# Optimization experiments

Hardware: AMD Instinct MI355X
Metric: run time of the kernel (lower is better)

The kernel has to match this reference:

```python
import jax, jax.numpy as jnp
import numpy as np

NEG_SLOPE = 0.2  # PyG GATv2Conv default negative_slope


def gatv2_conv(x, src, dst, Wl, bl, Wr, br, att, bias, concat=True):
    # x: [N, Fin]; src/dst: [E] (message flows src -> dst, softmax over dst)
    N = x.shape[0]
    H, C = att.shape
    xl = (x @ Wl + bl).reshape(N, H, C)  # source-side transform (lin_l)
    xr = (x @ Wr + br).reshape(N, H, C)  # target-side transform (lin_r)
    e = xl[src] + xr[dst]                              # [E, H, C]
    score = jnp.sum(jax.nn.leaky_relu(e, NEG_SLOPE) * att, axis=-1)  # [E, H]
    # segment softmax over incoming edges of each target node
    m = jax.ops.segment_max(score, dst, num_segments=N)               # [N, H]
    a = jnp.exp(score - m[dst])
    denom = jax.ops.segment_sum(a, dst, num_segments=N)               # [N, H]
    alpha = a / denom[dst]                                            # [E, H]
    out = jax.ops.segment_sum(xl[src] * alpha[..., None], dst, num_segments=N)  # [N, H, C]
    if concat:
        out = out.reshape(N, H * C)
    else:
        out = out.mean(axis=1)
    return out + bias


def setup_inputs() -> dict:
    key = jax.random.key(0)
    ks = jax.random.split(key, 12)
    N, E, Fin = 100000, 1600000, 128
    H1, C1 = 8, 16
    C2 = 64
    def glorot(k, shape):
        fan_in, fan_out = shape[0], shape[-1]
        lim = (6.0 / (fan_in + fan_out)) ** 0.5
        return jax.random.uniform(k, shape, jnp.float32, -lim, lim)
    x = jax.random.normal(ks[0], (N, Fin), jnp.float32)
    edge_index = jax.random.randint(ks[1], (2, E), 0, N, dtype=jnp.int64)
    return {
        "x": x,
        "edge_index": edge_index,
        "Wl1": glorot(ks[2], (Fin, H1 * C1)),
        "bl1": jnp.zeros((H1 * C1,), jnp.float32),
        "Wr1": glorot(ks[3], (Fin, H1 * C1)),
        "br1": jnp.zeros((H1 * C1,), jnp.float32),
        "att1": glorot(ks[4], (H1, C1)),
        "bias1": jnp.zeros((H1 * C1,), jnp.float32),
        "Wl2": glorot(ks[5], (H1 * C1, C2)),
        "bl2": jnp.zeros((C2,), jnp.float32),
        "Wr2": glorot(ks[6], (H1 * C1, C2)),
        "br2": jnp.zeros((C2,), jnp.float32),
        "att2": glorot(ks[7], (1, C2)),
        "bias2": jnp.zeros((C2,), jnp.float32),
    }


def reference(x, edge_index, Wl1, bl1, Wr1, br1, att1, bias1,
              Wl2, bl2, Wr2, br2, att2, bias2):
    N = x.shape[0]
    loops = jnp.arange(N, dtype=edge_index.dtype)
    src = jnp.concatenate([edge_index[0], loops])  # PyG adds self loops by default
    dst = jnp.concatenate([edge_index[1], loops])
    # eval mode: F.dropout(training=False) is identity
    h = gatv2_conv(x, src, dst, Wl1, bl1, Wr1, br1, att1, bias1, concat=True)
    h = jax.nn.elu(h)
    out = gatv2_conv(h, src, dst, Wl2, bl2, Wr2, br2, att2, bias2, concat=True)
    return out
```

## Files before the change

### kernel.cpp

```cpp
#include <hip/hip_runtime.h>
#include <math.h>

#define FIN 128
#define F1  128
#define C2  64
#define NEG 0.2f

#define BKT_SHIFT 8
#define BKT_SIZE  256
#define SCAT_CHUNK 8192
#define IMGCAP 8192

typedef _Float16 half4 __attribute__((ext_vector_type(4)));
typedef _Float16 f16x8 __attribute__((ext_vector_type(8)));
typedef _Float16 h2    __attribute__((ext_vector_type(2)));
typedef float    f32x4 __attribute__((ext_vector_type(4)));

union H8u { f16x8 v; h2 p[4]; };

__device__ __forceinline__ float lrelu(float z) { return fmaxf(z, NEG * z); }

__global__ __launch_bounds__(256) void bucket_hist_kernel(
    const int* __restrict__ ei, int* __restrict__ bcnt, int E, int ET, int NBKT) {
  __shared__ int sh[512];
  const int t = threadIdx.x;
  for (int b = t; b < NBKT; b += 256) sh[b] = 0;
  __syncthreads();
  const int g0 = blockIdx.x * SCAT_CHUNK + t;
#pragma unroll
  for (int i = 0; i < 32; ++i) {
    const int g = g0 + i * 256;
    if (g < ET) {
      const int dst = (g < E) ? ei[E + g] : (g - E);
      atomicAdd(&sh[dst >> BKT_SHIFT], 1);
    }
  }
  __syncthreads();
  for (int b = t; b < NBKT; b += 256)
    if (sh[b]) atomicAdd(&bcnt[b], sh[b]);
}

__global__ __launch_bounds__(512) void bucket_scan_kernel(
    const int* __restrict__ bcnt, int* __restrict__ bbase, int* __restrict__ bcur,
    int* __restrict__ indptr, int NBKT, int N, int ET) {
  __shared__ int sh[512];
  const int t = threadIdx.x;
  const int v = (t < NBKT) ? bcnt[t] : 0;
  sh[t] = v;
  __syncthreads();
  for (int off = 1; off < 512; off <<= 1) {
    int val = (t >= off) ? sh[t - off] : 0;
    __syncthreads();
    sh[t] += val;
    __syncthreads();
  }
  const int excl = sh[t] - v;
  if (t < NBKT) { bbase[t] = excl; bcur[t] = excl; }
  if (t == NBKT - 1) bbase[NBKT] = excl + v;
  if (t == 0) indptr[N] = ET;
}

__global__ __launch_bounds__(256) void bucket_scatter_kernel(
    const int* __restrict__ ei, int* __restrict__ bcur, int* __restrict__ tmp,
    int E, int ET, int NBKT) {
  __shared__ int sh_hist[512];
  __shared__ int sh_base[512];
  const int t = threadIdx.x;
  for (int b = t; b < NBKT; b += 256) sh_hist[b] = 0;
  __syncthreads();
  const int g0 = blockIdx.x * SCAT_CHUNK + t;
  int bk[32], pk[32];
#pragma unroll
  for (int i = 0; i < 32; ++i) {
    const int g = g0 + i * 256;
    int b = -1, p = 0;
    if (g < ET) {
      const int src = (g < E) ? ei[g] : (g - E);
      const int dst = (g < E) ? ei[E + g] : (g - E);
      b = dst >> BKT_SHIFT;
      p = (src << BKT_SHIFT) | (dst & (BKT_SIZE - 1));
      atomicAdd(&sh_hist[b], 1);
    }
    bk[i] = b; pk[i] = p;
  }
  __syncthreads();
  for (int b = t; b < NBKT; b += 256) {
    const int c = sh_hist[b];
    sh_base[b] = c ? atomicAdd(&bcur[b], c) : 0;
    sh_hist[b] = 0;
  }
  __syncthreads();
#pragma unroll
  for (int i = 0; i < 32; ++i) {
    if (bk[i] >= 0) {
      const int off = atomicAdd(&sh_hist[bk[i]], 1);
      tmp[sh_base[bk[i]] + off] = pk[i];
    }
  }
}

__global__ __launch_bounds__(256) void build_csr_kernel(
    const int* __restrict__ tmp, const int* __restrict__ bbase,
    int* __restrict__ indptr, int* __restrict__ csr, int N) {
  __shared__ int cnt[256];
  __shared__ int cur[256];
  __shared__ int img[IMGCAP];
  const int b = blockIdx.x;
  const int t = threadIdx.x;
  const int base = bbase[b];
  const int cntb = bbase[b + 1] - base;
  cnt[t] = 0;
  __syncthreads();
  for (int i = t; i < cntb; i += 256)
    atomicAdd(&cnt[tmp[base + i] & (BKT_SIZE - 1)], 1);
  __syncthreads();
  const int v = cnt[t];
  cur[t] = v;
  __syncthreads();
  for (int off = 1; off < 256; off <<= 1) {
    int val = (t >= off) ? cur[t - off] : 0;
    __syncthreads();
    cur[t] += val;
    __syncthreads();
  }
  const int excl = cur[t] - v;
  const int node = (b << BKT_SHIFT) + t;
  if (node < N) indptr[node] = base + excl;
  __syncthreads();
  cur[t] = excl;
  __syncthreads();
  if (cntb <= IMGCAP) {
    for (int i = t; i < cntb; i += 256) {
      const int p = tmp[base + i];
      const int pos = atomicAdd(&cur[p & (BKT_SIZE - 1)], 1);
      img[pos] = p >> BKT_SHIFT;
    }
    __syncthreads();
    for (int i = t; i < cntb; i += 256) csr[base + i] = img[i];
  } else {
    for (int i = t; i < cntb; i += 256) {
      const int p = tmp[base + i];
      const int pos = atomicAdd(&cur[p & (BKT_SIZE - 1)], 1);
      csr[base + pos] = p >> BKT_SHIFT;
    }
  }
}

__global__ __launch_bounds__(256) void conv_fp16_kernel(
    const float* __restrict__ src, _Float16* __restrict__ dst, int n4) {
  const int i = blockIdx.x * 256 + threadIdx.x;
  if (i < n4) {
    const float4 v = ((const float4*)src)[i];
    half4 h;
    h.x = (_Float16)v.x; h.y = (_Float16)v.y;
    h.z = (_Float16)v.z; h.w = (_Float16)v.w;
    ((half4*)dst)[i] = h;
  }
}

__global__ __launch_bounds__(256) void wtrans_kernel(
    const float* __restrict__ W0, const float* __restrict__ W1,
    const float* __restrict__ W2, const float* __restrict__ W3,
    _Float16* __restrict__ T0, _Float16* __restrict__ T1,
    _Float16* __restrict__ T2, _Float16* __restrict__ T3) {
  const int m = blockIdx.y;
  const float* W = (m == 0) ? W0 : (m == 1) ? W1 : (m == 2) ? W2 : W3;
  _Float16* T = (m == 0) ? T0 : (m == 1) ? T1 : (m == 2) ? T2 : T3;
  const int ncols = (m < 2) ? 128 : 64;
  const int idx = blockIdx.x * 256 + threadIdx.x;
  if (idx < ncols * 128) {
    const int n = idx >> 7;
    const int k = idx & 127;
    T[idx] = (_Float16)W[k * ncols + n];
  }
}

template<int NCOLS, int CPW>
__global__ __launch_bounds__(256) void gemm_mfma_kernel(
    const _Float16* __restrict__ A,
    const _Float16* __restrict__ Wt0, const float* __restrict__ b0, _Float16* __restrict__ O0,
    const _Float16* __restrict__ Wt1, const float* __restrict__ b1, _Float16* __restrict__ O1,
    int M) {
  const int zsel = blockIdx.z;
  const _Float16* Wt = zsel ? Wt1 : Wt0;
  const float* bias  = zsel ? b1 : b0;
  _Float16* O        = zsel ? O1 : O0;
  const int wave = threadIdx.x >> 6;
  const int lane = threadIdx.x & 63;
  const int row16 = lane & 15;
  const int quad  = lane >> 4;
  const int kb = quad * 8;
  f16x8 bfrag[CPW][4];
  float bv[CPW];
#pragma unroll
  for (int c = 0; c < CPW; ++c) {
    const int n0 = (wave * CPW + c) * 16;
    bv[c] = bias[n0 + row16];
#pragma unroll
    for (int kt = 0; kt < 4; ++kt)
      bfrag[c][kt] = *(const f16x8*)(Wt + (n0 + row16) * 128 + kt * 32 + kb);
  }
  const int rowTiles = (M + 15) >> 4;
  for (int rt = blockIdx.x; rt < rowTiles; rt += gridDim.x) {
    const int r0 = rt << 4;
    const int arow = min(r0 + row16, M - 1);
    f16x8 afrag[4];
#pragma unroll
    for (int kt = 0; kt < 4; ++kt)
      afrag[kt] = *(const f16x8*)(A + (size_t)arow * 128 + kt * 32 + kb);
    f32x4 acc[CPW];
#pragma unroll
    for (int c = 0; c < CPW; ++c) acc[c] = (f32x4){0.f, 0.f, 0.f, 0.f};
#pragma unroll
    for (int kt = 0; kt < 4; ++kt)
#pragma unroll
      for (int c = 0; c < CPW; ++c)
        acc[c] = __builtin_amdgcn_mfma_f32_16x16x32_f16(afrag[kt], bfrag[c][kt], acc[c], 0, 0, 0);
#pragma unroll
    for (int c = 0; c < CPW; ++c) {
      const int col = (wave * CPW + c) * 16 + row16;
#pragma unroll
      for (int r = 0; r < 4; ++r) {
        const int row = r0 + quad * 4 + r;
        if (row < M)
          O[(size_t)row * NCOLS + col] = (_Float16)(acc[c][r] + bv[c]);
      }
    }
  }
}

__global__ __launch_bounds__(256) void attn1_kernel(
    const _Float16* __restrict__ xl, const _Float16* __restrict__ xr,
    const float* __restrict__ att, const float* __restrict__ bias,
    const int* __restrict__ indptr, const int* __restrict__ csr,
    _Float16* __restrict__ hout, int N) {
  const int lane = threadIdx.x & 15;
  const int v = blockIdx.x * 16 + (threadIdx.x >> 4);
  if (v >= N) return;
  const int c8 = lane << 3;
  const _Float16* xlp = xl + c8;
  H8u xru; xru.v = *(const f16x8*)(xr + (v << 7) + c8);
  H8u atu;
  {
    const float4 a0 = *(const float4*)(att + c8);
    const float4 a1 = *(const float4*)(att + c8 + 4);
    f16x8 a;
    a[0] = (_Float16)a0.x; a[1] = (_Float16)a0.y; a[2] = (_Float16)a0.z; a[3] = (_Float16)a0.w;
    a[4] = (_Float16)a1.x; a[5] = (_Float16)a1.y; a[6] = (_Float16)a1.z; a[7] = (_Float16)a1.w;
    atu.v = a;
  }
  const h2 neg2 = {(_Float16)NEG, (_Float16)NEG};
  const h2 zero2 = {(_Float16)0.f, (_Float16)0.f};
  const int beg = indptr[v];
  const int end = indptr[v + 1];
  float l = 0.f;
  float acc[8] = {0.f, 0.f, 0.f, 0.f, 0.f, 0.f, 0.f, 0.f};
  int e = beg;
  for (; e + 4 <= end; e += 4) {
    const int s0 = csr[e + 0];
    const int s1 = csr[e + 1];
    const int s2 = csr[e + 2];
    const int s3 = csr[e + 3];
    H8u x0, x1, x2, x3;
    x0.v = *(const f16x8*)(xlp + (s0 << 7));
    x1.v = *(const f16x8*)(xlp + (s1 << 7));
    x2.v = *(const f16x8*)(xlp + (s2 << 7));
    x3.v = *(const f16x8*)(xlp + (s3 << 7));
    h2 sa0 = zero2, sa1 = zero2, sa2 = zero2, sa3 = zero2;
#pragma unroll
    for (int j = 0; j < 4; ++j) {
      h2 e0 = x0.p[j] + xru.p[j];
      h2 e1 = x1.p[j] + xru.p[j];
      h2 e2 = x2.p[j] + xru.p[j];
      h2 e3 = x3.p[j] + xru.p[j];
      e0 = __builtin_elementwise_max(e0, e0 * neg2);
      e1 = __builtin_elementwise_max(e1, e1 * neg2);
      e2 = __builtin_elementwise_max(e2, e2 * neg2);
      e3 = __builtin_elementwise_max(e3, e3 * neg2);
      sa0 = e0 * atu.p[j] + sa0;
      sa1 = e1 * atu.p[j] + sa1;
      sa2 = e2 * atu.p[j] + sa2;
      sa3 = e3 * atu.p[j] + sa3;
    }
    float t0 = (float)sa0[0] + (float)sa0[1];
    float t1 = (float)sa1[0] + (float)sa1[1];
    float t2 = (float)sa2[0] + (float)sa2[1];
    float t3 = (float)sa3[0] + (float)sa3[1];
    t0 += __shfl_xor(t0, 1);  t1 += __shfl_xor(t1, 1);
    t2 += __shfl_xor(t2, 1);  t3 += __shfl_xor(t3, 1);
    const float p0 = __expf(t0);
    const float p1 = __expf(t1);
    const float p2 = __expf(t2);
    const float p3 = __expf(t3);
    l += (p0 + p1) + (p2 + p3);
#pragma unroll
    for (int j = 0; j < 4; ++j) {
      acc[2*j]   = fmaf(p0, (float)x0.p[j][0], acc[2*j]);
      acc[2*j+1] = fmaf(p0, (float)x0.p[j][1], acc[2*j+1]);
      acc[2*j]   = fmaf(p1, (float)x1.p[j][0], acc[2*j]);
      acc[2*j+1] = fmaf(p1, (float)x1.p[j][1], acc[2*j+1]);
      acc[2*j]   = fmaf(p2, (float)x2.p[j][0], acc[2*j]);
      acc[2*j+1] = fmaf(p2, (float)x2.p[j][1], acc[2*j+1]);
      acc[2*j]   = fmaf(p3, (float)x3.p[j][0], acc[2*j]);
      acc[2*j+1] = fmaf(p3, (float)x3.p[j][1], acc[2*j+1]);
    }
  }
  for (; e < end; ++e) {
    const int s = csr[e];
    H8u xv; xv.v = *(const f16x8*)(xlp + (s << 7));
    h2 sa = zero2;
#pragma unroll
    for (int j = 0; j < 4; ++j) {
      h2 ev = xv.p[j] + xru.p[j];
      ev = __builtin_elementwise_max(ev, ev * neg2);
      sa = ev * atu.p[j] + sa;
    }
    float tt = (float)sa[0] + (float)sa[1];
    tt += __shfl_xor(tt, 1);
    const float p = __expf(tt);
    l += p;
#pragma unroll
    for (int j = 0; j < 4; ++j) {
      acc[2*j]   = fmaf(p, (float)xv.p[j][0], acc[2*j]);
      acc[2*j+1] = fmaf(p, (float)xv.p[j][1], acc[2*j+1]);
    }
  }
  const float rl = 1.f / l;
  const float4 b0 = *(const float4*)(bias + c8);
  const float4 b1 = *(const float4*)(bias + c8 + 4);
  float r[8];
  r[0] = fmaf(acc[0], rl, b0.x); r[1] = fmaf(acc[1], rl, b0.y);
  r[2] = fmaf(acc[2], rl, b0.z); r[3] = fmaf(acc[3], rl, b0.w);
  r[4] = fmaf(acc[4], rl, b1.x); r[5] = fmaf(acc[5], rl, b1.y);
  r[6] = fmaf(acc[6], rl, b1.z); r[7] = fmaf(acc[7], rl, b1.w);
  f16x8 hres;
#pragma unroll
  for (int i = 0; i < 8; ++i) {
    const float z = r[i] > 0.f ? r[i] : expm1f(r[i]);
    hres[i] = (_Float16)z;
  }
  *(f16x8*)(hout + (v << 7) + c8) = hres;
}

__global__ __launch_bounds__(256) void attn2_kernel(
    const _Float16* __restrict__ xl, const _Float16* __restrict__ xr,
    const float* __restrict__ att, const float* __restrict__ bias,
    const int* __restrict__ indptr, const int* __restrict__ csr,
    float* __restrict__ out, int N) {
  const int lane = threadIdx.x & 7;
  const int v = blockIdx.x * 32 + (threadIdx.x >> 3);
  if (v >= N) return;
  const int c8 = lane << 3;
  const _Float16* xlp = xl + c8;
  H8u xru; xru.v = *(const f16x8*)(xr + (v << 6) + c8);
  H8u atu;
  {
    const float4 a0 = *(const float4*)(att + c8);
    const float4 a1 = *(const float4*)(att + c8 + 4);
    f16x8 a;
    a[0] = (_Float16)a0.x; a[1] = (_Float16)a0.y; a[2] = (_Float16)a0.z; a[3] = (_Float16)a0.w;
    a[4] = (_Float16)a1.x; a[5] = (_Float16)a1.y; a[6] = (_Float16)a1.z; a[7] = (_Float16)a1.w;
    atu.v = a;
  }
  const h2 neg2 = {(_Float16)NEG, (_Float16)NEG};
  const h2 zero2 = {(_Float16)0.f, (_Float16)0.f};
  const int beg = indptr[v];
  const int end = indptr[v + 1];
  float l = 0.f;
  float acc[8] = {0.f, 0.f, 0.f, 0.f, 0.f, 0.f, 0.f, 0.f};
  int e = beg;
  for (; e + 4 <= end; e += 4) {
    const int s0 = csr[e + 0];
    const int s1 = csr[e + 1];
    const int s2 = csr[e + 2];
    const int s3 = csr[e + 3];
    H8u x0, x1, x2, x3;
    x0.v = *(const f16x8*)(xlp + (s0 << 6));
    x1.v = *(const f16x8*)(xlp + (s1 << 6));
    x2.v = *(const f16x8*)(xlp + (s2 << 6));
    x3.v = *(const f16x8*)(xlp + (s3 << 6));
    h2 sa0 = zero2, sa1 = zero2, sa2 = zero2, sa3 = zero2;
#pragma unroll
    for (int j = 0; j < 4; ++j) {
      h2 e0 = x0.p[j] + xru.p[j];
      h2 e1 = x1.p[j] + xru.p[j];
      h2 e2 = x2.p[j] + xru.p[j];
      h2 e3 = x3.p[j] + xru.p[j];
      e0 = __builtin_elementwise_max(e0, e0 * neg2);
      e1 = __builtin_elementwise_max(e1, e1 * neg2);
      e2 = __builtin_elementwise_max(e2, e2 * neg2);
      e3 = __builtin_elementwise_max(e3, e3 * neg2);
      sa0 = e0 * atu.p[j] + sa0;
      sa1 = e1 * atu.p[j] + sa1;
      sa2 = e2 * atu.p[j] + sa2;
      sa3 = e3 * atu.p[j] + sa3;
    }
    float t0 = (float)sa0[0] + (float)sa0[1];
    float t1 = (float)sa1[0] + (float)sa1[1];
    float t2 = (float)sa2[0] + (float)sa2[1];
    float t3 = (float)sa3[0] + (float)sa3[1];
    t0 += __shfl_xor(t0, 1);  t1 += __shfl_xor(t1, 1);
    t2 += __shfl_xor(t2, 1);  t3 += __shfl_xor(t3, 1);
    t0 += __shfl_xor(t0, 2);  t1 += __shfl_xor(t1, 2);
    t2 += __shfl_xor(t2, 2);  t3 += __shfl_xor(t3, 2);
    t0 += __shfl_xor(t0, 4);  t1 += __shfl_xor(t1, 4);
    t2 += __shfl_xor(t2, 4);  t3 += __shfl_xor(t3, 4);
    const float p0 = __expf(t0);
    const float p1 = __expf(t1);
    const float p2 = __expf(t2);
    const float p3 = __expf(t3);
    l += (p0 + p1) + (p2 + p3);
#pragma unroll
    for (int j = 0; j < 4; ++j) {
      acc[2*j]   = fmaf(p0, (float)x0.p[j][0], acc[2*j]);
      acc[2*j+1] = fmaf(p0, (float)x0.p[j][1], acc[2*j+1]);
      acc[2*j]   = fmaf(p1, (float)x1.p[j][0], acc[2*j]);
      acc[2*j+1] = fmaf(p1, (float)x1.p[j][1], acc[2*j+1]);
      acc[2*j]   = fmaf(p2, (float)x2.p[j][0], acc[2*j]);
      acc[2*j+1] = fmaf(p2, (float)x2.p[j][1], acc[2*j+1]);
      acc[2*j]   = fmaf(p3, (float)x3.p[j][0], acc[2*j]);
      acc[2*j+1] = fmaf(p3, (float)x3.p[j][1], acc[2*j+1]);
    }
  }
  for (; e < end; ++e) {
    const int s = csr[e];
    H8u xv; xv.v = *(const f16x8*)(xlp + (s << 6));
    h2 sa = zero2;
#pragma unroll
    for (int j = 0; j < 4; ++j) {
      h2 ev = xv.p[j] + xru.p[j];
      ev = __builtin_elementwise_max(ev, ev * neg2);
      sa = ev * atu.p[j] + sa;
    }
    float tt = (float)sa[0] + (float)sa[1];
    tt += __shfl_xor(tt, 1);
    tt += __shfl_xor(tt, 2);
    tt += __shfl_xor(tt, 4);
    const float p = __expf(tt);
    l += p;
#pragma unroll
    for (int j = 0; j < 4; ++j) {
      acc[2*j]   = fmaf(p, (float)xv.p[j][0], acc[2*j]);
      acc[2*j+1] = fmaf(p, (float)xv.p[j][1], acc[2*j+1]);
    }
  }
  const float rl = 1.f / l;
  const float4 b0 = *(const float4*)(bias + c8);
  const float4 b1 = *(const float4*)(bias + c8 + 4);
  float4 o0, o1;
  o0.x = fmaf(acc[0], rl, b0.x); o0.y = fmaf(acc[1], rl, b0.y);
  o0.z = fmaf(acc[2], rl, b0.z); o0.w = fmaf(acc[3], rl, b0.w);
  o1.x = fmaf(acc[4], rl, b1.x); o1.y = fmaf(acc[5], rl, b1.y);
  o1.z = fmaf(acc[6], rl, b1.z); o1.w = fmaf(acc[7], rl, b1.w);
  *(float4*)(out + (v << 6) + c8) = o0;
  *(float4*)(out + (v << 6) + c8 + 4) = o1;
}

extern "C" void kernel_launch(void* const* d_in, const int* in_sizes, int n_in,
                              void* d_out, int out_size, void* d_ws, size_t ws_size,
                              hipStream_t stream) {
  const float* x     = (const float*)d_in[0];
  const int*   ei    = (const int*)d_in[1];
  const float* Wl1   = (const float*)d_in[2];
  const float* bl1   = (const float*)d_in[3];
  const float* Wr1   = (const float*)d_in[4];
  const float* br1   = (const float*)d_in[5];
  const float* att1  = (const float*)d_in[6];
  const float* bias1 = (const float*)d_in[7];
  const float* Wl2   = (const float*)d_in[8];
  const float* bl2   = (const float*)d_in[9];
  const float* Wr2   = (const float*)d_in[10];
  const float* br2   = (const float*)d_in[11];
  const float* att2  = (const float*)d_in[12];
  const float* bias2 = (const float*)d_in[13];

  const int N  = in_sizes[0] / FIN;
  const int E  = in_sizes[1] / 2;
  const int ET = E + N;
  const int NBKT = (N + BKT_SIZE - 1) >> BKT_SHIFT;

  _Float16* xh    = (_Float16*)d_ws;
  _Float16* xl1h  = xh + (size_t)N * FIN;
  _Float16* xr1h  = xl1h + (size_t)N * F1;
  _Float16* hbufh = xr1h + (size_t)N * F1;
  _Float16* Wt1l  = hbufh + (size_t)N * F1;
  _Float16* Wt1r  = Wt1l + 128 * 128;
  _Float16* Wt2l  = Wt1r + 128 * 128;
  _Float16* Wt2r  = Wt2l + 64 * 128;
  int* indptr = (int*)(Wt2r + 64 * 128);
  int* csr    = indptr + (N + 1);
  int* bcnt   = csr + ET;
  int* bbase  = bcnt + 512;
  int* bcur   = bbase + 513;
  int* tmp    = (int*)hbufh;
  _Float16* xl2h = xl1h;
  _Float16* xr2h = xr1h;
  float* out  = (float*)d_out;

  const int sblocks = (ET + SCAT_CHUNK - 1) / SCAT_CHUNK;

  hipMemsetAsync(bcnt, 0, 512 * sizeof(int), stream);
  bucket_hist_kernel<<<sblocks, 256, 0, stream>>>(ei, bcnt, E, ET, NBKT);
  bucket_scan_kernel<<<1, 512, 0, stream>>>(bcnt, bbase, bcur, indptr, NBKT, N, ET);
  bucket_scatter_kernel<<<sblocks, 256, 0, stream>>>(ei, bcur, tmp, E, ET, NBKT);
  build_csr_kernel<<<NBKT, 256, 0, stream>>>(tmp, bbase, indptr, csr, N);

  const int n4 = N * FIN / 4;
  conv_fp16_kernel<<<(n4 + 255) / 256, 256, 0, stream>>>(x, xh, n4);
  wtrans_kernel<<<dim3(64, 4), 256, 0, stream>>>(Wl1, Wr1, Wl2, Wr2, Wt1l, Wt1r, Wt2l, Wt2r);

  gemm_mfma_kernel<128, 2><<<dim3(1024, 1, 2), 256, 0, stream>>>(
      xh, Wt1l, bl1, xl1h, Wt1r, br1, xr1h, N);

  attn1_kernel<<<(N + 15) / 16, 256, 0, stream>>>(xl1h, xr1h, att1, bias1, indptr, csr, hbufh, N);

  gemm_mfma_kernel<64, 1><<<dim3(1024, 1, 2), 256, 0, stream>>>(
      hbufh, Wt2l, bl2, xl2h, Wt2r, br2, xr2h, N);

  attn2_kernel<<<(N + 31) / 32, 256, 0, stream>>>(xl2h, xr2h, att2, bias2, indptr, csr, out, N);
}
```

Baseline: 358.9 us.

## Fuse fp32-to-fp16 conversion into GEMM, merge prep kernels, unroll attention by 8

The separate x-to-fp16 conversion kernel is removed. The first GEMM now loads fp32 rows and converts them in registers, which avoids writing and re-reading an fp16 copy of x. The weight transpose is merged into the bucket histogram kernel to save a launch. The attention kernels gain an 8-edge unrolled loop so more gathers are in flight, and they round the partial score to fp16 before the shuffle. The first GEMM now reads twice the bytes of A, and the wider unroll raises register pressure.

```diff
diff --git a/kernel.cpp b/kernel.cpp
--- a/kernel.cpp
+++ b/kernel.cpp
@@ -18,26 +18,40 @@
 
 union H8u { f16x8 v; h2 p[4]; };
 
-__device__ __forceinline__ float lrelu(float z) { return fmaxf(z, NEG * z); }
-
-__global__ __launch_bounds__(256) void bucket_hist_kernel(
-    const int* __restrict__ ei, int* __restrict__ bcnt, int E, int ET, int NBKT) {
-  __shared__ int sh[512];
+__global__ __launch_bounds__(256) void prep_kernel(
+    const int* __restrict__ ei, int* __restrict__ bcnt, int E, int ET, int NBKT, int sblocks,
+    const float* __restrict__ W0, const float* __restrict__ W1,
+    const float* __restrict__ W2, const float* __restrict__ W3,
+    _Float16* __restrict__ T0, _Float16* __restrict__ T1,
+    _Float16* __restrict__ T2, _Float16* __restrict__ T3) {
   const int t = threadIdx.x;
-  for (int b = t; b < NBKT; b += 256) sh[b] = 0;
-  __syncthreads();
-  const int g0 = blockIdx.x * SCAT_CHUNK + t;
-#pragma unroll
-  for (int i = 0; i < 32; ++i) {
-    const int g = g0 + i * 256;
-    if (g < ET) {
-      const int dst = (g < E) ? ei[E + g] : (g - E);
-      atomicAdd(&sh[dst >> BKT_SHIFT], 1);
-    }
-  }
-  __syncthreads();
-  for (int b = t; b < NBKT; b += 256)
-    if (sh[b]) atomicAdd(&bcnt[b], sh[b]);
+  if ((int)blockIdx.x < sblocks) {
+    __shared__ int sh[512];
+    for (int b = t; b < NBKT; b += 256) sh[b] = 0;
+    __syncthreads();
+    const int g0 = blockIdx.x * SCAT_CHUNK + t;
+#pragma unroll
+    for (int i = 0; i < 32; ++i) {
+      const int g = g0 + i * 256;
+      if (g < ET) {
+        const int dst = (g < E) ? ei[E + g] : (g - E);
+        atomicAdd(&sh[dst >> BKT_SHIFT], 1);
+      }
+    }
+    __syncthreads();
+    for (int b = t; b < NBKT; b += 256)
+      if (sh[b]) atomicAdd(&bcnt[b], sh[b]);
+  } else {
+    const int idx = ((int)blockIdx.x - sblocks) * 256 + t;
+    const float* W; _Float16* T; int local, ncols;
+    if (idx < 16384)      { W = W0; T = T0; local = idx;        ncols = 128; }
+    else if (idx < 32768) { W = W1; T = T1; local = idx-16384;  ncols = 128; }
+    else if (idx < 40960) { W = W2; T = T2; local = idx-32768;  ncols = 64;  }
+    else                  { W = W3; T = T3; local = idx-40960;  ncols = 64;  }
+    const int n = local >> 7;
+    const int k = local & 127;
+    T[local] = (_Float16)W[k * ncols + n];
+  }
 }
 
 __global__ __launch_bounds__(512) void bucket_scan_kernel(
@@ -146,41 +160,14 @@
   }
 }
 
-__global__ __launch_bounds__(256) void conv_fp16_kernel(
-    const float* __restrict__ src, _Float16* __restrict__ dst, int n4) {
-  const int i = blockIdx.x * 256 + threadIdx.x;
-  if (i < n4) {
-    const float4 v = ((const float4*)src)[i];
-    half4 h;
-    h.x = (_Float16)v.x; h.y = (_Float16)v.y;
-    h.z = (_Float16)v.z; h.w = (_Float16)v.w;
-    ((half4*)dst)[i] = h;
-  }
-}
-
-__global__ __launch_bounds__(256) void wtrans_kernel(
-    const float* __restrict__ W0, const float* __restrict__ W1,
-    const float* __restrict__ W2, const float* __restrict__ W3,
-    _Float16* __restrict__ T0, _Float16* __restrict__ T1,
-    _Float16* __restrict__ T2, _Float16* __restrict__ T3) {
-  const int m = blockIdx.y;
-  const float* W = (m == 0) ? W0 : (m == 1) ? W1 : (m == 2) ? W2 : W3;
-  _Float16* T = (m == 0) ? T0 : (m == 1) ? T1 : (m == 2) ? T2 : T3;
-  const int ncols = (m < 2) ? 128 : 64;
-  const int idx = blockIdx.x * 256 + threadIdx.x;
-  if (idx < ncols * 128) {
-    const int n = idx >> 7;
-    const int k = idx & 127;
-    T[idx] = (_Float16)W[k * ncols + n];
-  }
-}
-
-template<int NCOLS, int CPW>
+template<int NCOLS, int CPW, bool AF32>
 __global__ __launch_bounds__(256) void gemm_mfma_kernel(
-    const _Float16* __restrict__ A,
+    const void* __restrict__ Av,
     const _Float16* __restrict__ Wt0, const float* __restrict__ b0, _Float16* __restrict__ O0,
     const _Float16* __restrict__ Wt1, const float* __restrict__ b1, _Float16* __restrict__ O1,
     int M) {
+  const _Float16* A16 = (const _Float16*)Av;
+  const float*    A32 = (const float*)Av;
   const int zsel = blockIdx.z;
   const _Float16* Wt = zsel ? Wt1 : Wt0;
   const float* bias  = zsel ? b1 : b0;
@@ -205,9 +192,21 @@
     const int r0 = rt << 4;
     const int arow = min(r0 + row16, M - 1);
     f16x8 afrag[4];
-#pragma unroll
-    for (int kt = 0; kt < 4; ++kt)
-      afrag[kt] = *(const f16x8*)(A + (size_t)arow * 128 + kt * 32 + kb);
+    if (AF32) {
+#pragma unroll
+      for (int kt = 0; kt < 4; ++kt) {
+        const float4 u = *(const float4*)(A32 + (size_t)arow * 128 + kt * 32 + kb);
+        const float4 w = *(const float4*)(A32 + (size_t)arow * 128 + kt * 32 + kb + 4);
+        f16x8 f;
+        f[0] = (_Float16)u.x; f[1] = (_Float16)u.y; f[2] = (_Float16)u.z; f[3] = (_Float16)u.w;
+        f[4] = (_Float16)w.x; f[5] = (_Float16)w.y; f[6] = (_Float16)w.z; f[7] = (_Float16)w.w;
+        afrag[kt] = f;
+      }
+    } else {
+#pragma unroll
+      for (int kt = 0; kt < 4; ++kt)
+        afrag[kt] = *(const f16x8*)(A16 + (size_t)arow * 128 + kt * 32 + kb);
+    }
     f32x4 acc[CPW];
 #pragma unroll
     for (int c = 0; c < CPW; ++c) acc[c] = (f32x4){0.f, 0.f, 0.f, 0.f};
@@ -256,53 +255,62 @@
   float l = 0.f;
   float acc[8] = {0.f, 0.f, 0.f, 0.f, 0.f, 0.f, 0.f, 0.f};
   int e = beg;
+  for (; e + 8 <= end; e += 8) {
+    int s[8];
+#pragma unroll
+    for (int i = 0; i < 8; ++i) s[i] = csr[e + i];
+    H8u xv[8];
+#pragma unroll
+    for (int i = 0; i < 8; ++i) xv[i].v = *(const f16x8*)(xlp + (s[i] << 7));
+    float p[8];
+#pragma unroll
+    for (int i = 0; i < 8; ++i) {
+      h2 sa = zero2;
+#pragma unroll
+      for (int j = 0; j < 4; ++j) {
+        h2 ev = xv[i].p[j] + xru.p[j];
+        ev = __builtin_elementwise_max(ev, ev * neg2);
+        sa = ev * atu.p[j] + sa;
+      }
+      float tt = (float)(_Float16)(sa[0] + sa[1]);
+      tt += __shfl_xor(tt, 1);
+      p[i] = __expf(tt);
+    }
+#pragma unroll
+    for (int i = 0; i < 8; ++i) {
+      l += p[i];
+#pragma unroll
+      for (int j = 0; j < 4; ++j) {
+        acc[2*j]   = fmaf(p[i], (float)xv[i].p[j][0], acc[2*j]);
+        acc[2*j+1] = fmaf(p[i], (float)xv[i].p[j][1], acc[2*j+1]);
+      }
+    }
+  }
   for (; e + 4 <= end; e += 4) {
-    const int s0 = csr[e + 0];
-    const int s1 = csr[e + 1];
-    const int s2 = csr[e + 2];
-    const int s3 = csr[e + 3];
-    H8u x0, x1, x2, x3;
-    x0.v = *(const f16x8*)(xlp + (s0 << 7));
-    x1.v = *(const f16x8*)(xlp + (s1 << 7));
-    x2.v = *(const f16x8*)(xlp + (s2 << 7));
-    x3.v = *(const f16x8*)(xlp + (s3 << 7));
-    h2 sa0 = zero2, sa1 = zero2, sa2 = zero2, sa3 = zero2;
-#pragma unroll
-    for (int j = 0; j < 4; ++j) {
-      h2 e0 = x0.p[j] + xru.p[j];
-      h2 e1 = x1.p[j] + xru.p[j];
-      h2 e2 = x2.p[j] + xru.p[j];
-      h2 e3 = x3.p[j] + xru.p[j];
-      e0 = __builtin_elementwise_max(e0, e0 * neg2);
-      e1 = __builtin_elementwise_max(e1, e1 * neg2);
-      e2 = __builtin_elementwise_max(e2, e2 * neg2);
-      e3 = __builtin_elementwise_max(e3, e3 * neg2);
-      sa0 = e0 * atu.p[j] + sa0;
-      sa1 = e1 * atu.p[j] + sa1;
-      sa2 = e2 * atu.p[j] + sa2;
-      sa3 = e3 * atu.p[j] + sa3;
-    }
-    float t0 = (float)sa0[0] + (float)sa0[1];
-    float t1 = (float)sa1[0] + (float)sa1[1];
-    float t2 = (float)sa2[0] + (float)sa2[1];
-    float t3 = (float)sa3[0] + (float)sa3[1];
-    t0 += __shfl_xor(t0, 1);  t1 += __shfl_xor(t1, 1);
-    t2 += __shfl_xor(t2, 1);  t3 += __shfl_xor(t3, 1);
-    const float p0 = __expf(t0);
-    const float p1 = __expf(t1);
-    const float p2 = __expf(t2);
-    const float p3 = __expf(t3);
-    l += (p0 + p1) + (p2 + p3);
-#pragma unroll
-    for (int j = 0; j < 4; ++j) {
-      acc[2*j]   = fmaf(p0, (float)x0.p[j][0], acc[2*j]);
-      acc[2*j+1] = fmaf(p0, (float)x0.p[j][1], acc[2*j+1]);
-      acc[2*j]   = fmaf(p1, (float)x1.p[j][0], acc[2*j]);
-      acc[2*j+1] = fmaf(p1, (float)x1.p[j][1], acc[2*j+1]);
-      acc[2*j]   = fmaf(p2, (float)x2.p[j][0], acc[2*j]);
-      acc[2*j+1] = fmaf(p2, (float)x2.p[j][1], acc[2*j+1]);
-      acc[2*j]   = fmaf(p3, (float)x3.p[j][0], acc[2*j]);
-      acc[2*j+1] = fmaf(p3, (float)x3.p[j][1], acc[2*j+1]);
+    int s[4];
+#pragma unroll
+    for (int i = 0; i < 4; ++i) s[i] = csr[e + i];
+    H8u xv[4];
+#pragma unroll
+    for (int i = 0; i < 4; ++i) xv[i].v = *(const f16x8*)(xlp + (s[i] << 7));
+#pragma unroll
+    for (int i = 0; i < 4; ++i) {
+      h2 sa = zero2;
+#pragma unroll
+      for (int j = 0; j < 4; ++j) {
+        h2 ev = xv[i].p[j] + xru.p[j];
+        ev = __builtin_elementwise_max(ev, ev * neg2);
+        sa = ev * atu.p[j] + sa;
+      }
+      float tt = (float)(_Float16)(sa[0] + sa[1]);
+      tt += __shfl_xor(tt, 1);
+      const float p = __expf(tt);
+      l += p;
+#pragma unroll
+      for (int j = 0; j < 4; ++j) {
+        acc[2*j]   = fmaf(p, (float)xv[i].p[j][0], acc[2*j]);
+        acc[2*j+1] = fmaf(p, (float)xv[i].p[j][1], acc[2*j+1]);
+      }
     }
   }
   for (; e < end; ++e) {
@@ -315,7 +323,7 @@
       ev = __builtin_elementwise_max(ev, ev * neg2);
       sa = ev * atu.p[j] + sa;
     }
-    float tt = (float)sa[0] + (float)sa[1];
+    float tt = (float)(_Float16)(sa[0] + sa[1]);
     tt += __shfl_xor(tt, 1);
     const float p = __expf(tt);
     l += p;
@@ -369,57 +377,66 @@
   float l = 0.f;
   float acc[8] = {0.f, 0.f, 0.f, 0.f, 0.f, 0.f, 0.f, 0.f};
   int e = beg;
+  for (; e + 8 <= end; e += 8) {
+    int s[8];
+#pragma unroll
+    for (int i = 0; i < 8; ++i) s[i] = csr[e + i];
+    H8u xv[8];
+#pragma unroll
+    for (int i = 0; i < 8; ++i) xv[i].v = *(const f16x8*)(xlp + (s[i] << 6));
+    float p[8];
+#pragma unroll
+    for (int i = 0; i < 8; ++i) {
+      h2 sa = zero2;
+#pragma unroll
+      for (int j = 0; j < 4; ++j) {
+        h2 ev = xv[i].p[j] + xru.p[j];
+        ev = __builtin_elementwise_max(ev, ev * neg2);
+        sa = ev * atu.p[j] + sa;
+      }
+      float tt = (float)(_Float16)(sa[0] + sa[1]);
+      tt += __shfl_xor(tt, 1);
+      tt += __shfl_xor(tt, 2);
+      tt += __shfl_xor(tt, 4);
+      p[i] = __expf(tt);
+    }
+#pragma unroll
+    for (int i = 0; i < 8; ++i) {
+      l += p[i];
+#pragma unroll
+      for (int j = 0; j < 4; ++j) {
+        acc[2*j]   = fmaf(p[i], (float)xv[i].p[j][0], acc[2*j]);
+        acc[2*j+1] = fmaf(p[i], (float)xv[i].p[j][1], acc[2*j+1]);
+      }
+    }
+  }
   for (; e + 4 <= end; e += 4) {
-    const int s0 = csr[e + 0];
-    const int s1 = csr[e + 1];
-    const int s2 = csr[e + 2];
-    const int s3 = csr[e + 3];
-    H8u x0, x1, x2, x3;
-    x0.v = *(const f16x8*)(xlp + (s0 << 6));
-    x1.v = *(const f16x8*)(xlp + (s1 << 6));
-    x2.v = *(const f16x8*)(xlp + (s2 << 6));
-    x3.v = *(const f16x8*)(xlp + (s3 << 6));
-    h2 sa0 = zero2, sa1 = zero2, sa2 = zero2, sa3 = zero2;
-#pragma unroll
-    for (int j = 0; j < 4; ++j) {
-      h2 e0 = x0.p[j] + xru.p[j];
-      h2 e1 = x1.p[j] + xru.p[j];
-      h2 e2 = x2.p[j] + xru.p[j];
-      h2 e3 = x3.p[j] + xru.p[j];
-      e0 = __builtin_elementwise_max(e0, e0 * neg2);
-      e1 = __builtin_elementwise_max(e1, e1 * neg2);
-      e2 = __builtin_elementwise_max(e2, e2 * neg2);
-      e3 = __builtin_elementwise_max(e3, e3 * neg2);
-      sa0 = e0 * atu.p[j] + sa0;
-      sa1 = e1 * atu.p[j] + sa1;
-      sa2 = e2 * atu.p[j] + sa2;
-      sa3 = e3 * atu.p[j] + sa3;
-    }
-    float t0 = (float)sa0[0] + (float)sa0[1];
-    float t1 = (float)sa1[0] + (float)sa1[1];
-    float t2 = (float)sa2[0] + (float)sa2[1];
-    float t3 = (float)sa3[0] + (float)sa3[1];
-    t0 += __shfl_xor(t0, 1);  t1 += __shfl_xor(t1, 1);
-    t2 += __shfl_xor(t2, 1);  t3 += __shfl_xor(t3, 1);
-    t0 += __shfl_xor(t0, 2);  t1 += __shfl_xor(t1, 2);
-    t2 += __shfl_xor(t2, 2);  t3 += __shfl_xor(t3, 2);
-    t0 += __shfl_xor(t0, 4);  t1 += __shfl_xor(t1, 4);
-    t2 += __shfl_xor(t2, 4);  t3 += __shfl_xor(t3, 4);
-    const float p0 = __expf(t0);
-    const float p1 = __expf(t1);
-    const float p2 = __expf(t2);
-    const float p3 = __expf(t3);
-    l += (p0 + p1) + (p2 + p3);
-#pragma unroll
-    for (int j = 0; j < 4; ++j) {
-      acc[2*j]   = fmaf(p0, (float)x0.p[j][0], acc[2*j]);
-      acc[2*j+1] = fmaf(p0, (float)x0.p[j][1], acc[2*j+1]);
-      acc[2*j]   = fmaf(p1, (float)x1.p[j][0], acc[2*j]);
-      acc[2*j+1] = fmaf(p1, (float)x1.p[j][1], acc[2*j+1]);
-      acc[2*j]   = fmaf(p2, (float)x2.p[j][0], acc[2*j]);
-      acc[2*j+1] = fmaf(p2, (float)x2.p[j][1], acc[2*j+1]);
-      acc[2*j]   = fmaf(p3, (float)x3.p[j][0], acc[2*j]);
-      acc[2*j+1] = fmaf(p3, (float)x3.p[j][1], acc[2*j+1]);
+    int s[4];
+#pragma unroll
+    for (int i = 0; i < 4; ++i) s[i] = csr[e + i];
+    H8u xv[4];
+#pragma unroll
+    for (int i = 0; i < 4; ++i) xv[i].v = *(const f16x8*)(xlp + (s[i] << 6));
+#pragma unroll
+    for (int i = 0; i < 4; ++i) {
+      h2 sa = zero2;
+#pragma unroll
+      for (int j = 0; j < 4; ++j) {
+        h2 ev = xv[i].p[j] + xru.p[j];
+        ev = __builtin_elementwise_max(ev, ev * neg2);
+        sa = ev * atu.p[j] + sa;
+      }
+      float tt = (float)(_Float16)(sa[0] + sa[1]);
+      tt += __shfl_xor(tt, 1);
+      tt += __shfl_xor(tt, 2);
+      tt += __shfl_xor(tt, 4);
+      const float p = __expf(tt);
+      l += p;
+#pragma unroll
+      for (int j = 0; j < 4; ++j) {
+        acc[2*j]   = fmaf(p, (float)xv[i].p[j][0], acc[2*j]);
+        acc[2*j+1] = fmaf(p, (float)xv[i].p[j][1], acc[2*j+1]);
+      }
     }
   }
   for (; e < end; ++e) {
@@ -432,7 +449,7 @@
       ev = __builtin_elementwise_max(ev, ev * neg2);
       sa = ev * atu.p[j] + sa;
     }
-    float tt = (float)sa[0] + (float)sa[1];
+    float tt = (float)(_Float16)(sa[0] + sa[1]);
     tt += __shfl_xor(tt, 1);
     tt += __shfl_xor(tt, 2);
     tt += __shfl_xor(tt, 4);
@@ -479,8 +496,7 @@
   const int ET = E + N;
   const int NBKT = (N + BKT_SIZE - 1) >> BKT_SHIFT;
 
-  _Float16* xh    = (_Float16*)d_ws;
-  _Float16* xl1h  = xh + (size_t)N * FIN;
+  _Float16* xl1h  = (_Float16*)d_ws;
   _Float16* xr1h  = xl1h + (size_t)N * F1;
   _Float16* hbufh = xr1h + (size_t)N * F1;
   _Float16* Wt1l  = hbufh + (size_t)N * F1;
@@ -498,23 +514,22 @@
   float* out  = (float*)d_out;
 
   const int sblocks = (ET + SCAT_CHUNK - 1) / SCAT_CHUNK;
+  const int wblocks = 49152 / 256;
 
   hipMemsetAsync(bcnt, 0, 512 * sizeof(int), stream);
-  bucket_hist_kernel<<<sblocks, 256, 0, stream>>>(ei, bcnt, E, ET, NBKT);
+  prep_kernel<<<sblocks + wblocks, 256, 0, stream>>>(
+      ei, bcnt, E, ET, NBKT, sblocks,
+      Wl1, Wr1, Wl2, Wr2, Wt1l, Wt1r, Wt2l, Wt2r);
   bucket_scan_kernel<<<1, 512, 0, stream>>>(bcnt, bbase, bcur, indptr, NBKT, N, ET);
   bucket_scatter_kernel<<<sblocks, 256, 0, stream>>>(ei, bcur, tmp, E, ET, NBKT);
   build_csr_kernel<<<NBKT, 256, 0, stream>>>(tmp, bbase, indptr, csr, N);
 
-  const int n4 = N * FIN / 4;
-  conv_fp16_kernel<<<(n4 + 255) / 256, 256, 0, stream>>>(x, xh, n4);
-  wtrans_kernel<<<dim3(64, 4), 256, 0, stream>>>(Wl1, Wr1, Wl2, Wr2, Wt1l, Wt1r, Wt2l, Wt2r);
-
-  gemm_mfma_kernel<128, 2><<<dim3(1024, 1, 2), 256, 0, stream>>>(
-      xh, Wt1l, bl1, xl1h, Wt1r, br1, xr1h, N);
+  gemm_mfma_kernel<128, 2, true><<<dim3(1024, 1, 2), 256, 0, stream>>>(
+      x, Wt1l, bl1, xl1h, Wt1r, br1, xr1h, N);
 
   attn1_kernel<<<(N + 15) / 16, 256, 0, stream>>>(xl1h, xr1h, att1, bias1, indptr, csr, hbufh, N);
 
-  gemm_mfma_kernel<64, 1><<<dim3(1024, 1, 2), 256, 0, stream>>>(
+  gemm_mfma_kernel<64, 1, false><<<dim3(1024, 1, 2), 256, 0, stream>>>(
       hbufh, Wt2l, bl2, xl2h, Wt2r, br2, xr2h, N);
 
   attn2_kernel<<<(N + 31) / 32, 256, 0, stream>>>(xl2h, xr2h, att2, bias2, indptr, csr, out, N);
```

Measured after the change: 373.6 us. 4.1% more time.
